# Kernel optimization log

Hardware: AMD Instinct MI355X
Metric: run time of the kernel (lower is better)

The kernel has to match this reference:

```python
import jax, jax.numpy as jnp
import numpy as np

Z, N = 14336, 4096  # down_proj: intermediate -> hidden (Llama-3-8B scale)


def setup_inputs() -> dict:
    key = jax.random.key(0)
    k1, k2 = jax.random.split(key)
    x = jax.random.normal(k1, (1, 1, Z), dtype=jnp.float32)  # decode-time GEMV input
    W_t = jax.random.normal(k2, (Z, N), dtype=jnp.float32) * 0.02  # W.T, contiguous [Z, N]
    thresh = jnp.array([0.9], dtype=jnp.float32)
    return {"x": x, "W_t": W_t, "thresh": thresh}


def reference(x, W_t, thresh):
    # W_norm = ||orig_W[:, z]||_2 = row norms of W_t, shape [Z]
    W_norm = jnp.linalg.norm(W_t, axis=1)
    # abs_mul_leq: keep input coord z iff |x_z| * W_norm_z >= thresh
    m = (jnp.abs(x) * W_norm) >= thresh  # [1, 1, Z]
    # y[n] = sum_z mask_z * x_z * W_t[z, n]  (gather-transposed GEMV)
    xm = jnp.where(m, x, jnp.zeros((), dtype=x.dtype))
    return jnp.einsum('bsz,zn->bsn', xm, W_t)  # [1, 1, N]
```

## Files before the change

kernel.cpp:

```cpp
#include <hip/hip_runtime.h>
#include <cmath>


#define ZDIM   14336
#define NDIM   4096
#define NF4    1024
#define ZCHUNK 28
#define NBLK   512
#define DEPTH  4

typedef const __attribute__((address_space(1))) float* gas_fp;
typedef __attribute__((address_space(3))) float* las_fp;

__global__ __launch_bounds__(256) void fused_norm_gemv(
    const float* __restrict__ x,
    const float* __restrict__ Wt,
    const float* __restrict__ thresh,
    float* __restrict__ part) {
  const int t    = threadIdx.x;
  const int lane = t & 63;
  const int wv   = t >> 6;
  const int z0   = blockIdx.x * ZCHUNK;

  __shared__ float ring[DEPTH][NDIM];
  __shared__ float xs[ZCHUNK];
  __shared__ float red[2][4];

  const float th = thresh[0];
  if (t < ZCHUNK) xs[t] = x[z0 + t];
  __syncthreads();

  const int soff = wv * 1024 + lane * 4;

#define STAGE(slot, zrow) do {                                               \
    const float* gsrc = Wt + (size_t)(zrow) * NDIM + soff;                   \
    float* ldst = &ring[slot][soff];                                         \
    __builtin_amdgcn_global_load_lds((gas_fp)(gsrc      ), (las_fp)(ldst      ), 16, 0, 0); \
    __builtin_amdgcn_global_load_lds((gas_fp)(gsrc + 256), (las_fp)(ldst + 256), 16, 0, 0); \
    __builtin_amdgcn_global_load_lds((gas_fp)(gsrc + 512), (las_fp)(ldst + 512), 16, 0, 0); \
    __builtin_amdgcn_global_load_lds((gas_fp)(gsrc + 768), (las_fp)(ldst + 768), 16, 0, 0); \
  } while (0)

  STAGE(0, z0 + 0);
  STAGE(1, z0 + 1);
  STAGE(2, z0 + 2);
  STAGE(3, z0 + 3);

  float4 acc0 = {0,0,0,0}, acc1 = {0,0,0,0}, acc2 = {0,0,0,0}, acc3 = {0,0,0,0};

#define ROW(r, VM, DO_STAGE) do {                                            \
    asm volatile("s_waitcnt vmcnt(" #VM ")" ::: "memory");                   \
    __builtin_amdgcn_s_barrier();                                            \
    asm volatile("" ::: "memory");                                           \
    const float4* r4 = (const float4*)&ring[(r) & (DEPTH - 1)][0];           \
    const float4 wa = r4[t], wb = r4[t + 256], wc = r4[t + 512], wd = r4[t + 768]; \
    float ssv = wa.x*wa.x + wa.y*wa.y + wa.z*wa.z + wa.w*wa.w                \
              + wb.x*wb.x + wb.y*wb.y + wb.z*wb.z + wb.w*wb.w                \
              + wc.x*wc.x + wc.y*wc.y + wc.z*wc.z + wc.w*wc.w                \
              + wd.x*wd.x + wd.y*wd.y + wd.z*wd.z + wd.w*wd.w;               \
    ssv += __shfl_xor(ssv, 1, 64);                                           \
    ssv += __shfl_xor(ssv, 2, 64);                                           \
    ssv += __shfl_xor(ssv, 4, 64);                                           \
    ssv += __shfl_xor(ssv, 8, 64);                                           \
    ssv += __shfl_xor(ssv, 16, 64);                                          \
    ssv += __shfl_xor(ssv, 32, 64);                                          \
    if (lane == 0) red[(r) & 1][wv] = ssv;                                   \
    asm volatile("s_waitcnt lgkmcnt(0)" ::: "memory");                       \
    __builtin_amdgcn_s_barrier();                                            \
    asm volatile("" ::: "memory");                                           \
    const float n2 = red[(r)&1][0] + red[(r)&1][1] + red[(r)&1][2] + red[(r)&1][3]; \
    const float xz = xs[r];                                                  \
    if (fabsf(xz) * sqrtf(n2) >= th) {              \
      acc0.x = fmaf(xz, wa.x, acc0.x); acc0.y = fmaf(xz, wa.y, acc0.y);      \
      acc0.z = fmaf(xz, wa.z, acc0.z); acc0.w = fmaf(xz, wa.w, acc0.w);      \
      acc1.x = fmaf(xz, wb.x, acc1.x); acc1.y = fmaf(xz, wb.y, acc1.y);      \
      acc1.z = fmaf(xz, wb.z, acc1.z); acc1.w = fmaf(xz, wb.w, acc1.w);      \
      acc2.x = fmaf(xz, wc.x, acc2.x); acc2.y = fmaf(xz, wc.y, acc2.y);      \
      acc2.z = fmaf(xz, wc.z, acc2.z); acc2.w = fmaf(xz, wc.w, acc2.w);      \
      acc3.x = fmaf(xz, wd.x, acc3.x); acc3.y = fmaf(xz, wd.y, acc3.y);      \
      acc3.z = fmaf(xz, wd.z, acc3.z); acc3.w = fmaf(xz, wd.w, acc3.w);      \
    }                                                                        \
    if (DO_STAGE) STAGE((r) & (DEPTH - 1), z0 + (r) + DEPTH);                \
  } while (0)

  #pragma unroll 4
  for (int r = 0; r < ZCHUNK - DEPTH; ++r) ROW(r, 12, 1);
  ROW(24, 12, 0);
  ROW(25, 8, 0);
  ROW(26, 4, 0);
  ROW(27, 0, 0);

  float4* p4 = (float4*)part + (size_t)blockIdx.x * NF4;
  p4[t]       = acc0;
  p4[t + 256] = acc1;
  p4[t + 512] = acc2;
  p4[t + 768] = acc3;
#undef ROW
#undef STAGE
}

__global__ __launch_bounds__(256) void reduce_parts(
    const float* __restrict__ part, float* __restrict__ y) {
  const int t  = threadIdx.x;
  const int c  = t & 3;
  const int jg = t >> 2;
  const int c4 = blockIdx.x * 4 + c;
  const float4* __restrict__ p4 = (const float4*)part;

  float4 s = {0.f, 0.f, 0.f, 0.f};
  #pragma unroll
  for (int jj = 0; jj < 8; ++jj) {
    const float4 v = p4[(size_t)(jg * 8 + jj) * NF4 + c4];
    s.x += v.x; s.y += v.y; s.z += v.z; s.w += v.w;
  }

  __shared__ float4 sh[64][4];
  sh[jg][c] = s;
  __syncthreads();
  if (jg < 8) {
    #pragma unroll
    for (int k = 1; k < 8; ++k) {
      const float4 v = sh[jg + 8 * k][c];
      s.x += v.x; s.y += v.y; s.z += v.z; s.w += v.w;
    }
    sh[jg][c] = s;
  }
  __syncthreads();
  if (jg == 0) {
    #pragma unroll
    for (int k = 1; k < 8; ++k) {
      const float4 v = sh[k][c];
      s.x += v.x; s.y += v.y; s.z += v.z; s.w += v.w;
    }
    ((float4*)y)[c4] = s;
  }
}

extern "C" void kernel_launch(void* const* d_in, const int* in_sizes, int n_in,
                              void* d_out, int out_size, void* d_ws, size_t ws_size,
                              hipStream_t stream) {
  const float* x      = (const float*)d_in[0];
  const float* Wt     = (const float*)d_in[1];
  const float* thresh = (const float*)d_in[2];
  float* y            = (float*)d_out;
  float* part         = (float*)d_ws;

  fused_norm_gemv<<<NBLK, 256, 0, stream>>>(x, Wt, thresh, part);
  reduce_parts<<<NF4 / 4, 256, 0, stream>>>(part, y);
}
```

Measured before the change: 44.33 us.

## Replace LDS ring staging with register-prefetched rows and a single barrier

Drops the asynchronous global-to-LDS ring buffer. Each thread now loads its weight row slices straight into registers, rotating through four register sets three rows ahead. The FMA for a row is deferred until its mask is known, so each row needs only one barrier instead of two. This is meant to remove the LDS round trip and a barrier per row, at the cost of more registers (launch bounds now ask for 2 blocks per CU) and one fewer row of data in flight.

```diff
diff --git a/kernel.cpp b/kernel.cpp
--- a/kernel.cpp
+++ b/kernel.cpp
@@ -7,12 +7,8 @@
 #define NF4    1024
 #define ZCHUNK 28
 #define NBLK   512
-#define DEPTH  4
 
-typedef const __attribute__((address_space(1))) float* gas_fp;
-typedef __attribute__((address_space(3))) float* las_fp;
-
-__global__ __launch_bounds__(256) void fused_norm_gemv(
+__global__ __launch_bounds__(256, 2) void fused_norm_gemv(
     const float* __restrict__ x,
     const float* __restrict__ Wt,
     const float* __restrict__ thresh,
@@ -22,73 +18,81 @@
   const int wv   = t >> 6;
   const int z0   = blockIdx.x * ZCHUNK;
 
-  __shared__ float ring[DEPTH][NDIM];
   __shared__ float xs[ZCHUNK];
   __shared__ float red[2][4];
 
-  const float th = thresh[0];
   if (t < ZCHUNK) xs[t] = x[z0 + t];
   __syncthreads();
+  const float th = thresh[0];
 
-  const int soff = wv * 1024 + lane * 4;
-
-#define STAGE(slot, zrow) do {                                               \
-    const float* gsrc = Wt + (size_t)(zrow) * NDIM + soff;                   \
-    float* ldst = &ring[slot][soff];                                         \
-    __builtin_amdgcn_global_load_lds((gas_fp)(gsrc      ), (las_fp)(ldst      ), 16, 0, 0); \
-    __builtin_amdgcn_global_load_lds((gas_fp)(gsrc + 256), (las_fp)(ldst + 256), 16, 0, 0); \
-    __builtin_amdgcn_global_load_lds((gas_fp)(gsrc + 512), (las_fp)(ldst + 512), 16, 0, 0); \
-    __builtin_amdgcn_global_load_lds((gas_fp)(gsrc + 768), (las_fp)(ldst + 768), 16, 0, 0); \
-  } while (0)
-
-  STAGE(0, z0 + 0);
-  STAGE(1, z0 + 1);
-  STAGE(2, z0 + 2);
-  STAGE(3, z0 + 3);
+  const float4* __restrict__ W4 = reinterpret_cast<const float4*>(Wt) + t;
 
   float4 acc0 = {0,0,0,0}, acc1 = {0,0,0,0}, acc2 = {0,0,0,0}, acc3 = {0,0,0,0};
 
-#define ROW(r, VM, DO_STAGE) do {                                            \
-    asm volatile("s_waitcnt vmcnt(" #VM ")" ::: "memory");                   \
-    __builtin_amdgcn_s_barrier();                                            \
-    asm volatile("" ::: "memory");                                           \
-    const float4* r4 = (const float4*)&ring[(r) & (DEPTH - 1)][0];           \
-    const float4 wa = r4[t], wb = r4[t + 256], wc = r4[t + 512], wd = r4[t + 768]; \
-    float ssv = wa.x*wa.x + wa.y*wa.y + wa.z*wa.z + wa.w*wa.w                \
-              + wb.x*wb.x + wb.y*wb.y + wb.z*wb.z + wb.w*wb.w                \
-              + wc.x*wc.x + wc.y*wc.y + wc.z*wc.z + wc.w*wc.w                \
-              + wd.x*wd.x + wd.y*wd.y + wd.z*wd.z + wd.w*wd.w;               \
-    ssv += __shfl_xor(ssv, 1, 64);                                           \
-    ssv += __shfl_xor(ssv, 2, 64);                                           \
-    ssv += __shfl_xor(ssv, 4, 64);                                           \
-    ssv += __shfl_xor(ssv, 8, 64);                                           \
-    ssv += __shfl_xor(ssv, 16, 64);                                          \
-    ssv += __shfl_xor(ssv, 32, 64);                                          \
-    if (lane == 0) red[(r) & 1][wv] = ssv;                                   \
+  float4 s0a,s0b,s0c,s0d, s1a,s1b,s1c,s1d, s2a,s2b,s2c,s2d, s3a,s3b,s3c,s3d;
+
+#define LOADROW(S, r) do {                                                   \
+    const float4* p_ = W4 + (size_t)(z0 + (r)) * NF4;                        \
+    S##a = p_[0]; S##b = p_[256]; S##c = p_[512]; S##d = p_[768];            \
+  } while (0)
+
+#define FMA16(S, xz) do {                                                    \
+    acc0.x = fmaf(xz, S##a.x, acc0.x); acc0.y = fmaf(xz, S##a.y, acc0.y);    \
+    acc0.z = fmaf(xz, S##a.z, acc0.z); acc0.w = fmaf(xz, S##a.w, acc0.w);    \
+    acc1.x = fmaf(xz, S##b.x, acc1.x); acc1.y = fmaf(xz, S##b.y, acc1.y);    \
+    acc1.z = fmaf(xz, S##b.z, acc1.z); acc1.w = fmaf(xz, S##b.w, acc1.w);    \
+    acc2.x = fmaf(xz, S##c.x, acc2.x); acc2.y = fmaf(xz, S##c.y, acc2.y);    \
+    acc2.z = fmaf(xz, S##c.z, acc2.z); acc2.w = fmaf(xz, S##c.w, acc2.w);    \
+    acc3.x = fmaf(xz, S##d.x, acc3.x); acc3.y = fmaf(xz, S##d.y, acc3.y);    \
+    acc3.z = fmaf(xz, S##d.z, acc3.z); acc3.w = fmaf(xz, S##d.w, acc3.w);    \
+  } while (0)
+
+#define ROW(CUR, PREV, r) do {                                               \
+    float ss = CUR##a.x*CUR##a.x + CUR##a.y*CUR##a.y                         \
+             + CUR##a.z*CUR##a.z + CUR##a.w*CUR##a.w                         \
+             + CUR##b.x*CUR##b.x + CUR##b.y*CUR##b.y                         \
+             + CUR##b.z*CUR##b.z + CUR##b.w*CUR##b.w                         \
+             + CUR##c.x*CUR##c.x + CUR##c.y*CUR##c.y                         \
+             + CUR##c.z*CUR##c.z + CUR##c.w*CUR##c.w                         \
+             + CUR##d.x*CUR##d.x + CUR##d.y*CUR##d.y                         \
+             + CUR##d.z*CUR##d.z + CUR##d.w*CUR##d.w;                        \
+    ss += __shfl_xor(ss, 1, 64);                                             \
+    ss += __shfl_xor(ss, 2, 64);                                             \
+    ss += __shfl_xor(ss, 4, 64);                                             \
+    ss += __shfl_xor(ss, 8, 64);                                             \
+    ss += __shfl_xor(ss, 16, 64);                                            \
+    ss += __shfl_xor(ss, 32, 64);                                            \
+    if (lane == 0) red[(r) & 1][wv] = ss;                                    \
+    if (mP) FMA16(PREV, xzP);                   \
+    if ((r) + 3 < ZCHUNK) LOADROW(PREV, (r) + 3);    \
     asm volatile("s_waitcnt lgkmcnt(0)" ::: "memory");                       \
     __builtin_amdgcn_s_barrier();                                            \
     asm volatile("" ::: "memory");                                           \
-    const float n2 = red[(r)&1][0] + red[(r)&1][1] + red[(r)&1][2] + red[(r)&1][3]; \
-    const float xz = xs[r];                                                  \
-    if (fabsf(xz) * sqrtf(n2) >= th) {              \
-      acc0.x = fmaf(xz, wa.x, acc0.x); acc0.y = fmaf(xz, wa.y, acc0.y);      \
-      acc0.z = fmaf(xz, wa.z, acc0.z); acc0.w = fmaf(xz, wa.w, acc0.w);      \
-      acc1.x = fmaf(xz, wb.x, acc1.x); acc1.y = fmaf(xz, wb.y, acc1.y);      \
-      acc1.z = fmaf(xz, wb.z, acc1.z); acc1.w = fmaf(xz, wb.w, acc1.w);      \
-      acc2.x = fmaf(xz, wc.x, acc2.x); acc2.y = fmaf(xz, wc.y, acc2.y);      \
-      acc2.z = fmaf(xz, wc.z, acc2.z); acc2.w = fmaf(xz, wc.w, acc2.w);      \
-      acc3.x = fmaf(xz, wd.x, acc3.x); acc3.y = fmaf(xz, wd.y, acc3.y);      \
-      acc3.z = fmaf(xz, wd.z, acc3.z); acc3.w = fmaf(xz, wd.w, acc3.w);      \
-    }                                                                        \
-    if (DO_STAGE) STAGE((r) & (DEPTH - 1), z0 + (r) + DEPTH);                \
+    const float n2 = red[(r) & 1][0] + red[(r) & 1][1]                       \
+                   + red[(r) & 1][2] + red[(r) & 1][3];                      \
+    const float xz = xs[(r)];                                                \
+    mP  = (fabsf(xz) * sqrtf(n2) >= th);                                     \
+    xzP = xz;                                                                \
   } while (0)
 
-  #pragma unroll 4
-  for (int r = 0; r < ZCHUNK - DEPTH; ++r) ROW(r, 12, 1);
-  ROW(24, 12, 0);
-  ROW(25, 8, 0);
-  ROW(26, 4, 0);
-  ROW(27, 0, 0);
+  LOADROW(s0, 0);
+  LOADROW(s1, 1);
+  LOADROW(s2, 2);
+
+  float xzP = 0.0f;
+  bool  mP  = false;
+
+  for (int rb = 0; rb < 24; rb += 4) {
+    ROW(s0, s3, rb + 0);
+    ROW(s1, s0, rb + 1);
+    ROW(s2, s1, rb + 2);
+    ROW(s3, s2, rb + 3);
+  }
+  ROW(s0, s3, 24);
+  ROW(s1, s0, 25);
+  ROW(s2, s1, 26);
+  ROW(s3, s2, 27);
+  if (mP) FMA16(s3, xzP);
 
   float4* p4 = (float4*)part + (size_t)blockIdx.x * NF4;
   p4[t]       = acc0;
@@ -96,7 +100,8 @@
   p4[t + 512] = acc2;
   p4[t + 768] = acc3;
 #undef ROW
-#undef STAGE
+#undef FMA16
+#undef LOADROW
 }
 
 __global__ __launch_bounds__(256) void reduce_parts(
```

Result: slower. 46.20 us (+4.2%).
